# Kernel tuning notes

Hardware: AMD Instinct MI355X
Metric: run time of the kernel (lower is better)

The kernel has to match this reference:

```python
import jax, jax.numpy as jnp
import numpy as np

N, M = 1024, 1024
GATES = ["ii", "hi", "if", "hf", "ig", "hg", "io", "ho"]


def setup_inputs() -> dict:
    key = jax.random.key(0)
    names = ["x", "h", "c"] + [f"{p}_{g}" for g in GATES for p in ("L", "R", "b")]
    keys = jax.random.split(key, len(names))
    out = {}
    for nm, k in zip(names, keys):
        if nm in ("x", "h", "c"):
            sh = (N, M)
            scale = 1.0
        else:
            p = nm.split("_")[0]
            sh = {"L": (N, N), "R": (M, M), "b": (N, M)}[p]
            scale = 0.05  # keep gate pre-activations in a sane range
        out[nm] = jax.random.normal(k, sh, dtype=jnp.float32) * scale
    return out


def _klin(L, R, b, x):
    # kronecker_addmm: left @ x @ right + bias
    return L @ x @ R + b


def reference(x, h, c,
              L_ii, R_ii, b_ii, L_hi, R_hi, b_hi,
              L_if, R_if, b_if, L_hf, R_hf, b_hf,
              L_ig, R_ig, b_ig, L_hg, R_hg, b_hg,
              L_io, R_io, b_io, L_ho, R_ho, b_ho):
    i = jax.nn.sigmoid(_klin(L_ii, R_ii, b_ii, x) + _klin(L_hi, R_hi, b_hi, h))
    f = jax.nn.sigmoid(_klin(L_if, R_if, b_if, x) + _klin(L_hf, R_hf, b_hf, h))
    g = jnp.tanh(_klin(L_ig, R_ig, b_ig, x) + _klin(L_hg, R_hg, b_hg, h))
    o = jax.nn.sigmoid(_klin(L_io, R_io, b_io, x) + _klin(L_ho, R_ho, b_ho, h))
    c_new = f * c + i * g
    h_new = o * jnp.tanh(c_new)
    return (h_new, c_new)
```

## Files before the change

### kernel.cpp

```cpp
#include <hip/hip_runtime.h>
#include <stdint.h>

typedef __bf16 bf16x8 __attribute__((ext_vector_type(8)));
typedef float  f32x4  __attribute__((ext_vector_type(4)));
typedef uint16_t u16;

#define MAT_ELEMS (1024 * 1024)
#define LDK 1024


__device__ __forceinline__ u16 to_bf16(float f) {
  union { float f; uint32_t u; } v; v.f = f;
  uint32_t u = v.u;
  uint32_t r = u + 0x7FFFu + ((u >> 16) & 1u);
  return (u16)(r >> 16);
}

__device__ __forceinline__ float bf16_to_f32(u16 b) {
  union { uint32_t u; float f; } v; v.u = ((uint32_t)b) << 16;
  return v.f;
}

__device__ __forceinline__ void gll16(const void* g, void* l) {
  __builtin_amdgcn_global_load_lds(
      (__attribute__((address_space(1))) void*)const_cast<void*>(g),
      (__attribute__((address_space(3))) void*)(l),
      16, 0, 0);
}

__device__ __forceinline__ float fast_sigmoid(float x) {
  x = fminf(fmaxf(x, -30.f), 30.f);
  return 1.0f / (1.0f + __expf(-x));
}

__device__ __forceinline__ float fast_tanh(float x) {
  x = fminf(fmaxf(x, -15.f), 15.f);
  float e = __expf(2.0f * x);
  return (e - 1.0f) / (e + 1.0f);
}


struct P8  { const float* p[8]; };
struct P10 { const float* p[10]; };
struct B8  { const float* b[8]; };

__global__ __launch_bounds__(256) void cast8_kernel(P8 s, u16* __restrict__ dst) {
  const float* src = s.p[blockIdx.y];
  u16* d = dst + ((size_t)blockIdx.y << 20);
  int i = (blockIdx.x * 256 + threadIdx.x) * 4;
  f32x4 v = *reinterpret_cast<const f32x4*>(src + i);
  ushort4 o;
  o.x = to_bf16(v[0]); o.y = to_bf16(v[1]);
  o.z = to_bf16(v[2]); o.w = to_bf16(v[3]);
  *reinterpret_cast<ushort4*>(d + i) = o;
}

__global__ __launch_bounds__(256) void transpose_cast_kernel(P10 s, u16* __restrict__ dstbase) {
  __shared__ float tile[32][33];
  const float* src = s.p[blockIdx.z];
  u16* dst = dstbase + ((size_t)blockIdx.z << 20);
  int tx = threadIdx.x & 31;
  int ty = threadIdx.x >> 5;
  int c0 = blockIdx.x * 32;
  int r0 = blockIdx.y * 32;
#pragma unroll
  for (int i = 0; i < 4; ++i)
    tile[ty + i * 8][tx] = src[(size_t)(r0 + ty + i * 8) * 1024 + c0 + tx];
  __syncthreads();
#pragma unroll
  for (int i = 0; i < 4; ++i) {
    int n = c0 + ty + i * 8;
    int k = r0 + tx;
    dst[(size_t)n * 1024 + k] = to_bf16(tile[tx][ty + i * 8]);
  }
}


template <int MODE>
__device__ __forceinline__ void gemm64_body(
    const u16* __restrict__ A, const u16* __restrict__ B,
    int row0, int col0,
    u16* __restrict__ out, const float* __restrict__ bias,
    u16* As, u16* Bs)
{
  const int tid  = threadIdx.x;
  const int lane = tid & 63;
  const int w    = tid >> 6;
  const int wr   = w >> 1;
  const int wc   = w & 1;
  const int r16  = lane & 15;
  const int kg   = lane >> 4;

  f32x4 acc[2][4];
#pragma unroll
  for (int m = 0; m < 2; ++m)
#pragma unroll
    for (int n = 0; n < 4; ++n) {
      f32x4 z = {0.f, 0.f, 0.f, 0.f};
      acc[m][n] = z;
    }

  const int srow = tid >> 2;
  const int skk  = (tid & 3) * 8;
  u16* lA  = As + srow * 32 + skk;
  u16* lB0 = Bs + srow * 32 + skk;
  u16* lB1 = Bs + (srow + 64) * 32 + skk;
  const u16* gA  = A + (size_t)(row0 + srow)      * LDK + skk;
  const u16* gB0 = B + (size_t)(col0 + srow)      * LDK + skk;
  const u16* gB1 = B + (size_t)(col0 + srow + 64) * LDK + skk;

  for (int kt = 0; kt < 32; ++kt) {
    __syncthreads();
    gll16(gA  + kt * 32, lA);
    gll16(gB0 + kt * 32, lB0);
    gll16(gB1 + kt * 32, lB1);
    __syncthreads();

    bf16x8 af[2], bfr[4];
#pragma unroll
    for (int m = 0; m < 2; ++m)
      af[m] = *reinterpret_cast<const bf16x8*>(As + (wr * 32 + m * 16 + r16) * 32 + kg * 8);
#pragma unroll
    for (int n = 0; n < 4; ++n)
      bfr[n] = *reinterpret_cast<const bf16x8*>(Bs + (wc * 64 + n * 16 + r16) * 32 + kg * 8);
#pragma unroll
    for (int m = 0; m < 2; ++m)
#pragma unroll
      for (int n = 0; n < 4; ++n)
        acc[m][n] = __builtin_amdgcn_mfma_f32_16x16x32_bf16(af[m], bfr[n], acc[m][n], 0, 0, 0);
  }

#pragma unroll
  for (int m = 0; m < 2; ++m) {
#pragma unroll
    for (int r = 0; r < 4; ++r) {
      int row = row0 + wr * 32 + m * 16 + kg * 4 + r;
#pragma unroll
      for (int n = 0; n < 4; ++n) {
        int col = col0 + wc * 64 + n * 16 + r16;
        size_t idx = (size_t)row * 1024 + col;
        float v = acc[m][n][r];
        if (MODE == 1) v += bias[idx];
        out[idx] = to_bf16(v);
      }
    }
  }
}

__global__ __launch_bounds__(256) void gemm_stage1_kernel(
    const u16* __restrict__ Lb, const u16* __restrict__ xT,
    const u16* __restrict__ hT, u16* __restrict__ Tbuf)
{
  __shared__ u16 As[64 * 32];
  __shared__ u16 Bs[128 * 32];
  int g = blockIdx.y;
  const u16* A = Lb + ((size_t)g << 20);
  const u16* B = (g & 1) ? hT : xT;
  int row0 = (blockIdx.x >> 3) * 64;
  int col0 = (blockIdx.x & 7) * 128;
  gemm64_body<0>(A, B, row0, col0, Tbuf + ((size_t)g << 20), nullptr, As, Bs);
}

__global__ __launch_bounds__(256) void gemm_stage2_kernel(
    const u16* __restrict__ Tbuf, const u16* __restrict__ RT,
    B8 bp, u16* __restrict__ P)
{
  __shared__ u16 As[64 * 32];
  __shared__ u16 Bs[128 * 32];
  int g = blockIdx.y;
  const u16* A = Tbuf + ((size_t)g << 20);
  const u16* B = RT   + ((size_t)g << 20);
  int row0 = (blockIdx.x >> 3) * 64;
  int col0 = (blockIdx.x & 7) * 128;
  gemm64_body<1>(A, B, row0, col0, P + ((size_t)g << 20), bp.b[g], As, Bs);
}

__global__ __launch_bounds__(256) void lstm_cell_kernel(
    const u16* __restrict__ P, const float* __restrict__ c, float* __restrict__ out)
{
  int i = (blockIdx.x * 256 + threadIdx.x) * 4;
  ushort4 pv[8];
#pragma unroll
  for (int g = 0; g < 8; ++g)
    pv[g] = *reinterpret_cast<const ushort4*>(P + (size_t)g * MAT_ELEMS + i);
  f32x4 cc = *reinterpret_cast<const f32x4*>(c + i);
  f32x4 hn, cn;
#pragma unroll
  for (int j = 0; j < 4; ++j) {
    float pi = bf16_to_f32((&pv[0].x)[j]) + bf16_to_f32((&pv[1].x)[j]);
    float pf = bf16_to_f32((&pv[2].x)[j]) + bf16_to_f32((&pv[3].x)[j]);
    float pg = bf16_to_f32((&pv[4].x)[j]) + bf16_to_f32((&pv[5].x)[j]);
    float po = bf16_to_f32((&pv[6].x)[j]) + bf16_to_f32((&pv[7].x)[j]);
    float ig = fast_sigmoid(pi);
    float fg = fast_sigmoid(pf);
    float gg = fast_tanh(pg);
    float og = fast_sigmoid(po);
    float cv = fg * cc[j] + ig * gg;
    cn[j] = cv;
    hn[j] = og * fast_tanh(cv);
  }
  *reinterpret_cast<f32x4*>(out + i) = hn;
  *reinterpret_cast<f32x4*>(out + MAT_ELEMS + i) = cn;
}


extern "C" void kernel_launch(void* const* d_in, const int* in_sizes, int n_in,
                              void* d_out, int out_size, void* d_ws, size_t ws_size,
                              hipStream_t stream) {
  const float* x = (const float*)d_in[0];
  const float* h = (const float*)d_in[1];
  const float* c = (const float*)d_in[2];

  u16* Lb   = (u16*)d_ws;
  u16* xT   = Lb + ((size_t)8 << 20);
  u16* hT   = xT + ((size_t)1 << 20);
  u16* RT   = hT + ((size_t)1 << 20);
  u16* Tbuf = RT + ((size_t)8 << 20);
  u16* P    = Tbuf + ((size_t)8 << 20);

  P8 lp;
  for (int g = 0; g < 8; ++g) lp.p[g] = (const float*)d_in[3 + 3 * g];
  P10 tp;
  tp.p[0] = x; tp.p[1] = h;
  for (int g = 0; g < 8; ++g) tp.p[2 + g] = (const float*)d_in[4 + 3 * g];
  B8 bp;
  for (int g = 0; g < 8; ++g) bp.b[g] = (const float*)d_in[5 + 3 * g];

  cast8_kernel<<<dim3(1024, 8), 256, 0, stream>>>(lp, Lb);
  transpose_cast_kernel<<<dim3(32, 32, 10), 256, 0, stream>>>(tp, xT);
  gemm_stage1_kernel<<<dim3(128, 8), 256, 0, stream>>>(Lb, xT, hT, Tbuf);
  gemm_stage2_kernel<<<dim3(128, 8), 256, 0, stream>>>(Tbuf, RT, bp, P);
  lstm_cell_kernel<<<1024, 256, 0, stream>>>(P, c, (float*)d_out);
}
```

Baseline: 251.5 us.

## Use 128x128 double-buffered GEMM tiles and move bias add into cell kernel

Both GEMM stages grow the block tile from 64x128 to 128x128 and use two LDS buffers, so the next K-slice's global-to-LDS loads are issued while MFMAs run on the current slice. This raises arithmetic per loaded byte and hides load latency. The bias add moves from the stage-2 epilogue into the LSTM cell kernel, which now reads the eight fp32 bias matrices. The risks are fewer blocks (512 across 8 gates), higher LDS and register use that lowers occupancy, and the bias now being added after bf16 rounding.

```diff
diff --git a/kernel.cpp b/kernel.cpp
--- a/kernel.cpp
+++ b/kernel.cpp
@@ -76,12 +76,10 @@
 }
 
 
-template <int MODE>
-__device__ __forceinline__ void gemm64_body(
+__device__ __forceinline__ void gemm128_dbuf(
     const u16* __restrict__ A, const u16* __restrict__ B,
-    int row0, int col0,
-    u16* __restrict__ out, const float* __restrict__ bias,
-    u16* As, u16* Bs)
+    int row0, int col0, u16* __restrict__ out,
+    u16* As0, u16* As1, u16* Bs0, u16* Bs1)
 {
   const int tid  = threadIdx.x;
   const int lane = tid & 63;
@@ -91,9 +89,9 @@
   const int r16  = lane & 15;
   const int kg   = lane >> 4;
 
-  f32x4 acc[2][4];
-#pragma unroll
-  for (int m = 0; m < 2; ++m)
+  f32x4 acc[4][4];
+#pragma unroll
+  for (int m = 0; m < 4; ++m)
 #pragma unroll
     for (int n = 0; n < 4; ++n) {
       f32x4 z = {0.f, 0.f, 0.f, 0.f};
@@ -102,46 +100,52 @@
 
   const int srow = tid >> 2;
   const int skk  = (tid & 3) * 8;
-  u16* lA  = As + srow * 32 + skk;
-  u16* lB0 = Bs + srow * 32 + skk;
-  u16* lB1 = Bs + (srow + 64) * 32 + skk;
-  const u16* gA  = A + (size_t)(row0 + srow)      * LDK + skk;
-  const u16* gB0 = B + (size_t)(col0 + srow)      * LDK + skk;
-  const u16* gB1 = B + (size_t)(col0 + srow + 64) * LDK + skk;
-
-  for (int kt = 0; kt < 32; ++kt) {
-    __syncthreads();
-    gll16(gA  + kt * 32, lA);
-    gll16(gB0 + kt * 32, lB0);
-    gll16(gB1 + kt * 32, lB1);
-    __syncthreads();
-
-    bf16x8 af[2], bfr[4];
-#pragma unroll
-    for (int m = 0; m < 2; ++m)
-      af[m] = *reinterpret_cast<const bf16x8*>(As + (wr * 32 + m * 16 + r16) * 32 + kg * 8);
+
+  auto stage = [&](u16* Asb, u16* Bsb, int kt) {
+    const u16* Ak = A + kt * 32 + skk;
+    const u16* Bk = B + kt * 32 + skk;
+    gll16(Ak + (size_t)(row0 + srow)      * LDK, Asb + srow * 32 + skk);
+    gll16(Ak + (size_t)(row0 + srow + 64) * LDK, Asb + (srow + 64) * 32 + skk);
+    gll16(Bk + (size_t)(col0 + srow)      * LDK, Bsb + srow * 32 + skk);
+    gll16(Bk + (size_t)(col0 + srow + 64) * LDK, Bsb + (srow + 64) * 32 + skk);
+  };
+
+  auto compute = [&](const u16* Asb, const u16* Bsb) {
+    bf16x8 af[4], bfr[4];
+#pragma unroll
+    for (int m = 0; m < 4; ++m)
+      af[m] = *reinterpret_cast<const bf16x8*>(Asb + (wr * 64 + m * 16 + r16) * 32 + kg * 8);
 #pragma unroll
     for (int n = 0; n < 4; ++n)
-      bfr[n] = *reinterpret_cast<const bf16x8*>(Bs + (wc * 64 + n * 16 + r16) * 32 + kg * 8);
-#pragma unroll
-    for (int m = 0; m < 2; ++m)
+      bfr[n] = *reinterpret_cast<const bf16x8*>(Bsb + (wc * 64 + n * 16 + r16) * 32 + kg * 8);
+#pragma unroll
+    for (int m = 0; m < 4; ++m)
 #pragma unroll
       for (int n = 0; n < 4; ++n)
         acc[m][n] = __builtin_amdgcn_mfma_f32_16x16x32_bf16(af[m], bfr[n], acc[m][n], 0, 0, 0);
-  }
-
-#pragma unroll
-  for (int m = 0; m < 2; ++m) {
+  };
+
+  stage(As0, Bs0, 0);
+  __syncthreads();
+
+  for (int kt = 0; kt < 32; kt += 2) {
+    stage(As1, Bs1, kt + 1);
+    compute(As0, Bs0);
+    __syncthreads();
+    if (kt + 2 < 32) stage(As0, Bs0, kt + 2);
+    compute(As1, Bs1);
+    __syncthreads();
+  }
+
+#pragma unroll
+  for (int m = 0; m < 4; ++m) {
 #pragma unroll
     for (int r = 0; r < 4; ++r) {
-      int row = row0 + wr * 32 + m * 16 + kg * 4 + r;
+      int row = row0 + wr * 64 + m * 16 + kg * 4 + r;
 #pragma unroll
       for (int n = 0; n < 4; ++n) {
         int col = col0 + wc * 64 + n * 16 + r16;
-        size_t idx = (size_t)row * 1024 + col;
-        float v = acc[m][n][r];
-        if (MODE == 1) v += bias[idx];
-        out[idx] = to_bf16(v);
+        out[(size_t)row * 1024 + col] = to_bf16(acc[m][n][r]);
       }
     }
   }
@@ -151,46 +155,51 @@
     const u16* __restrict__ Lb, const u16* __restrict__ xT,
     const u16* __restrict__ hT, u16* __restrict__ Tbuf)
 {
-  __shared__ u16 As[64 * 32];
-  __shared__ u16 Bs[128 * 32];
+  __shared__ u16 As0[128 * 32], As1[128 * 32];
+  __shared__ u16 Bs0[128 * 32], Bs1[128 * 32];
   int g = blockIdx.y;
   const u16* A = Lb + ((size_t)g << 20);
   const u16* B = (g & 1) ? hT : xT;
-  int row0 = (blockIdx.x >> 3) * 64;
+  int row0 = (blockIdx.x >> 3) * 128;
   int col0 = (blockIdx.x & 7) * 128;
-  gemm64_body<0>(A, B, row0, col0, Tbuf + ((size_t)g << 20), nullptr, As, Bs);
+  gemm128_dbuf(A, B, row0, col0, Tbuf + ((size_t)g << 20), As0, As1, Bs0, Bs1);
 }
 
 __global__ __launch_bounds__(256) void gemm_stage2_kernel(
     const u16* __restrict__ Tbuf, const u16* __restrict__ RT,
-    B8 bp, u16* __restrict__ P)
-{
-  __shared__ u16 As[64 * 32];
-  __shared__ u16 Bs[128 * 32];
+    u16* __restrict__ P)
+{
+  __shared__ u16 As0[128 * 32], As1[128 * 32];
+  __shared__ u16 Bs0[128 * 32], Bs1[128 * 32];
   int g = blockIdx.y;
   const u16* A = Tbuf + ((size_t)g << 20);
   const u16* B = RT   + ((size_t)g << 20);
-  int row0 = (blockIdx.x >> 3) * 64;
+  int row0 = (blockIdx.x >> 3) * 128;
   int col0 = (blockIdx.x & 7) * 128;
-  gemm64_body<1>(A, B, row0, col0, P + ((size_t)g << 20), bp.b[g], As, Bs);
+  gemm128_dbuf(A, B, row0, col0, P + ((size_t)g << 20), As0, As1, Bs0, Bs1);
 }
 
 __global__ __launch_bounds__(256) void lstm_cell_kernel(
-    const u16* __restrict__ P, const float* __restrict__ c, float* __restrict__ out)
+    const u16* __restrict__ P, B8 bp, const float* __restrict__ c,
+    float* __restrict__ out)
 {
   int i = (blockIdx.x * 256 + threadIdx.x) * 4;
   ushort4 pv[8];
 #pragma unroll
   for (int g = 0; g < 8; ++g)
     pv[g] = *reinterpret_cast<const ushort4*>(P + (size_t)g * MAT_ELEMS + i);
+  f32x4 bv[8];
+#pragma unroll
+  for (int g = 0; g < 8; ++g)
+    bv[g] = *reinterpret_cast<const f32x4*>(bp.b[g] + i);
   f32x4 cc = *reinterpret_cast<const f32x4*>(c + i);
   f32x4 hn, cn;
 #pragma unroll
   for (int j = 0; j < 4; ++j) {
-    float pi = bf16_to_f32((&pv[0].x)[j]) + bf16_to_f32((&pv[1].x)[j]);
-    float pf = bf16_to_f32((&pv[2].x)[j]) + bf16_to_f32((&pv[3].x)[j]);
-    float pg = bf16_to_f32((&pv[4].x)[j]) + bf16_to_f32((&pv[5].x)[j]);
-    float po = bf16_to_f32((&pv[6].x)[j]) + bf16_to_f32((&pv[7].x)[j]);
+    float pi = bf16_to_f32((&pv[0].x)[j]) + bf16_to_f32((&pv[1].x)[j]) + bv[0][j] + bv[1][j];
+    float pf = bf16_to_f32((&pv[2].x)[j]) + bf16_to_f32((&pv[3].x)[j]) + bv[2][j] + bv[3][j];
+    float pg = bf16_to_f32((&pv[4].x)[j]) + bf16_to_f32((&pv[5].x)[j]) + bv[4][j] + bv[5][j];
+    float po = bf16_to_f32((&pv[6].x)[j]) + bf16_to_f32((&pv[7].x)[j]) + bv[6][j] + bv[7][j];
     float ig = fast_sigmoid(pi);
     float fg = fast_sigmoid(pf);
     float gg = fast_tanh(pg);
@@ -228,7 +237,7 @@
 
   cast8_kernel<<<dim3(1024, 8), 256, 0, stream>>>(lp, Lb);
   transpose_cast_kernel<<<dim3(32, 32, 10), 256, 0, stream>>>(tp, xT);
-  gemm_stage1_kernel<<<dim3(128, 8), 256, 0, stream>>>(Lb, xT, hT, Tbuf);
-  gemm_stage2_kernel<<<dim3(128, 8), 256, 0, stream>>>(Tbuf, RT, bp, P);
-  lstm_cell_kernel<<<1024, 256, 0, stream>>>(P, c, (float*)d_out);
-}
+  gemm_stage1_kernel<<<dim3(64, 8), 256, 0, stream>>>(Lb, xT, hT, Tbuf);
+  gemm_stage2_kernel<<<dim3(64, 8), 256, 0, stream>>>(Tbuf, RT, P);
+  lstm_cell_kernel<<<1024, 256, 0, stream>>>(P, bp, c, (float*)d_out);
+}
```

After: 240.4 us. 4.4% less time.
